# Optimization experiments

Measured on AMD Instinct MI355X. Metric: run time of the kernel, lower is better.

## Reference

```python
import jax, jax.numpy as jnp
import numpy as np

BETA = 1e-8
ALPHA = 0.5
CHOOSE_K = 128
MEMORY_SIZE = 65536
KEY_DIM = 256
BATCH = 1024


def _l2norm(x, axis=-1, eps=1e-12):
    return x / jnp.sqrt(jnp.sum(x * x, axis=axis, keepdims=True) + eps)


def setup_inputs() -> dict:
    key = jax.random.key(0)
    k1, k2, k3 = jax.random.split(key, 3)
    q = _l2norm(jax.random.normal(k1, (BATCH, KEY_DIM), dtype=jnp.float32))
    memory_key = _l2norm(jax.random.normal(k2, (MEMORY_SIZE, KEY_DIM), dtype=jnp.float32))
    # module init: hist[:] = 1e-5; add small random variation so topk is non-degenerate
    memory_hist = 1e-5 + 1e-3 * jax.random.uniform(k3, (MEMORY_SIZE,), dtype=jnp.float32)
    # module init: values = ones, second half zeroed
    memory_values = jnp.concatenate([
        jnp.ones((MEMORY_SIZE // 2,), dtype=jnp.float32),
        jnp.zeros((MEMORY_SIZE - MEMORY_SIZE // 2,), dtype=jnp.float32),
    ])
    return {"q": q, "memory_key": memory_key,
            "memory_hist": memory_hist, "memory_values": memory_values}


def reference(q, memory_key, memory_hist, memory_values):
    # obtain_topk over FULL memory: dense similarity [B, M]
    sims = jnp.matmul(q, memory_key.T)                      # [B, M]
    scores = jnp.exp(sims - 1.0) * (memory_hist + BETA)[None, :]
    _, k_idxs = jax.lax.top_k(scores, CHOOSE_K)             # [B, K]

    # gather reduced memory at topk indices
    red_keys = memory_key[k_idxs]                           # [B, K, D]
    red_hist = memory_hist[k_idxs] * ALPHA                  # [B, K]
    red_vals = memory_values[k_idxs]                        # [B, K]

    # posterior over the K gathered slots
    sim_k = jnp.einsum('bd,bkd->bk', q, red_keys)           # [B, K]
    joint = jnp.exp(sim_k - 1.0) * (red_hist + BETA)        # [B, K]
    posterior = joint / jnp.sum(joint, axis=1, keepdims=True)
    result = jnp.sum(posterior * red_vals, axis=1)          # [B]
    return result
```

## Files before the change

kernel.cpp:

```cpp
#include <hip/hip_runtime.h>

#define BATCH   1024
#define MSIZE   65536
#define KDIM    256
#define CHOOSEK 128
#define SELK    160
#define BETA    1e-8f
#define ALPHA   0.5f
#define KSCALE  426666.7f

typedef short bf16x8 __attribute__((ext_vector_type(8)));
typedef float f32x4  __attribute__((ext_vector_type(4)));

__device__ inline unsigned int pack2bf(float a, float b) {
    unsigned int ua = __float_as_uint(a);
    unsigned int ub = __float_as_uint(b);
    ua += 0x7fffu + ((ua >> 16) & 1u);
    ub += 0x7fffu + ((ub >> 16) & 1u);
    return (ua >> 16) | (ub & 0xffff0000u);
}

#define GLD16(g, l) __builtin_amdgcn_global_load_lds( \
    (const __attribute__((address_space(1))) unsigned int*)(g), \
    (__attribute__((address_space(3))) unsigned int*)(l), 16, 0, 0)

__global__ __launch_bounds__(256)
void convert_kernel(const float* __restrict__ q, const float* __restrict__ key,
                    unsigned short* __restrict__ qb, unsigned short* __restrict__ kb)
{
    const int id = blockIdx.x * 256 + threadIdx.x;
    const float* src; unsigned short* dst; int off;
    if (blockIdx.x < 128) { src = q;   dst = qb; off = id; }
    else                  { src = key; dst = kb; off = id - 32768; }
    const float4* s4 = (const float4*)src;
    float4 a = s4[off * 2];
    float4 b = s4[off * 2 + 1];
    uint4 p = make_uint4(pack2bf(a.x, a.y), pack2bf(a.z, a.w),
                         pack2bf(b.x, b.y), pack2bf(b.z, b.w));
    ((uint4*)dst)[off] = p;
}

__global__ __launch_bounds__(256)
void score_kernel(const unsigned short* __restrict__ qb,
                  const unsigned short* __restrict__ kb,
                  const float* __restrict__ hist,
                  unsigned char* __restrict__ s8)
{
    __shared__ __align__(16) unsigned short As[2][128 * 32];
    __shared__ __align__(16) unsigned short Bs[2][128 * 32];
    const int tid = threadIdx.x;
    const int bid = blockIdx.x;
    const int b0 = ((bid >> 3) & 7) * 128;
    const int n0 = ((bid & 7) + ((bid >> 6) << 3)) * 128;
    const int lane = tid & 63, wave = tid >> 6;
    const int wm = (wave >> 1) * 64, wn = (wave & 1) * 64;
    const int l15 = lane & 15, l4 = lane >> 4;

    f32x4 acc[4][4] = {};

    const int srow = tid >> 2;
    const int seg  = (tid & 3) * 8;
    const unsigned short* gA = qb + (size_t)(b0 + srow) * KDIM + seg;
    const unsigned short* gB = kb + (size_t)(n0 + srow) * KDIM + seg;
    const int lofs = srow * 32 + seg;

    GLD16(gA,             &As[0][lofs]);
    GLD16(gA + 64 * KDIM, &As[0][lofs + 64 * 32]);
    GLD16(gB,             &Bs[0][lofs]);
    GLD16(gB + 64 * KDIM, &Bs[0][lofs + 64 * 32]);
    __syncthreads();

#pragma unroll
    for (int ks = 0; ks < 8; ++ks) {
        const int cur = ks & 1;
        if (ks < 7) {
            const int nxt = cur ^ 1;
            const int ko  = (ks + 1) * 32;
            GLD16(gA + ko,             &As[nxt][lofs]);
            GLD16(gA + ko + 64 * KDIM, &As[nxt][lofs + 64 * 32]);
            GLD16(gB + ko,             &Bs[nxt][lofs]);
            GLD16(gB + ko + 64 * KDIM, &Bs[nxt][lofs + 64 * 32]);
        }
        bf16x8 af[4], bfr[4];
#pragma unroll
        for (int i = 0; i < 4; ++i)
            af[i] = *(const bf16x8*)(&As[cur][(wm + i * 16 + l15) * 32 + l4 * 8]);
#pragma unroll
        for (int j = 0; j < 4; ++j)
            bfr[j] = *(const bf16x8*)(&Bs[cur][(wn + j * 16 + l15) * 32 + l4 * 8]);
#pragma unroll
        for (int i = 0; i < 4; ++i)
#pragma unroll
            for (int j = 0; j < 4; ++j)
                acc[i][j] = __builtin_amdgcn_mfma_f32_16x16x32_bf16(af[i], bfr[j], acc[i][j], 0, 0, 0);
        __syncthreads();
    }

    float hj[4];
#pragma unroll
    for (int j = 0; j < 4; ++j)
        hj[j] = (hist[n0 + wn + j * 16 + l15] + BETA) * KSCALE;
#pragma unroll
    for (int i = 0; i < 4; ++i) {
        const size_t rbase = (size_t)(b0 + wm + i * 16 + l4 * 4) * MSIZE;
#pragma unroll
        for (int j = 0; j < 4; ++j) {
            const int n = n0 + wn + j * 16 + l15;
#pragma unroll
            for (int reg = 0; reg < 4; ++reg) {
                float sc = __expf(acc[i][j][reg] - 1.0f) * hj[j];
                s8[rbase + (size_t)reg * MSIZE + n] = (unsigned char)(int)fminf(sc, 255.0f);
            }
        }
    }
}

__global__ __launch_bounds__(256, 4)
void select_kernel(const float* __restrict__ q,
                   const float* __restrict__ key,
                   const float* __restrict__ hist,
                   const float* __restrict__ vals,
                   const unsigned char* __restrict__ s8,
                   float* __restrict__ out)
{
    const int b   = blockIdx.x;
    const int tid = threadIdx.x;

    __shared__ __align__(16) float qs[KDIM];
    __shared__ unsigned int hcnt[16 * 257];
    __shared__ int   stot[256];
    __shared__ int   scal[2];
    __shared__ int   cidx[1024];
    __shared__ float csc[1024], cjj[1024], cjv[1024];
    __shared__ float wred[8];

    qs[tid] = q[(size_t)b * KDIM + tid];
    const uint4* rowp = reinterpret_cast<const uint4*>(s8 + (size_t)b * MSIZE);
    const int rep = (tid & 15) * 257;

    int H = -1;
    int minb = 128;
    for (;;) {
        for (int i = tid; i < 16 * 257; i += 256) hcnt[i] = 0u;
        if (tid == 0) { scal[0] = -1; scal[1] = 0; }
        __syncthreads();

        for (int i = 0; i < 16; ++i) {
            uint4 v = rowp[i * 256 + tid];
            unsigned int w[4] = {v.x, v.y, v.z, v.w};
#pragma unroll
            for (int k = 0; k < 4; ++k) {
                if (minb == 0 || (w[k] & 0x80808080u)) {
#pragma unroll
                    for (int jj = 0; jj < 4; ++jj) {
                        int bb = (int)((w[k] >> (8 * jj)) & 0xffu);
                        if (bb >= minb) atomicAdd(&hcnt[rep + bb], 1u);
                    }
                }
            }
        }
        __syncthreads();
        { unsigned int t = 0;
#pragma unroll
          for (int k = 0; k < 16; ++k) t += hcnt[k * 257 + tid];
          stot[tid] = (int)t; }
        __syncthreads();

        if (tid < 64) {
            const int l = tid;
            int t0 = stot[l * 4], t1 = stot[l * 4 + 1], t2 = stot[l * 4 + 2], t3 = stot[l * 4 + 3];
            int lsum = t0 + t1 + t2 + t3;
            int s = lsum;
#pragma unroll
            for (int off = 1; off < 64; off <<= 1) {
                int u = __shfl_down(s, off, 64);
                if (l + off < 64) s += u;
            }
            int A  = s - lsum;
            int S3 = A + t3;
            int S2 = S3 + t2;
            int S1 = S2 + t1;
            int S0 = S1 + t0;
            if (S0 >= SELK && S1 < SELK) scal[0] = l * 4 + 0;
            if (S1 >= SELK && S2 < SELK) scal[0] = l * 4 + 1;
            if (S2 >= SELK && S3 < SELK) scal[0] = l * 4 + 2;
            if (S3 >= SELK && A  < SELK) scal[0] = l * 4 + 3;
        }
        __syncthreads();
        H = scal[0];
        __syncthreads();
        if (H >= 0) break;
        minb = 0;
    }

    const unsigned int uH = (unsigned int)H;
    const bool pre = (H >= 128);
    for (int i = 0; i < 16; ++i) {
        uint4 v = rowp[i * 256 + tid];
        const int base = (i * 256 + tid) * 16;
        unsigned int w[4] = {v.x, v.y, v.z, v.w};
#pragma unroll
        for (int k = 0; k < 4; ++k) {
            if (!pre || (w[k] & 0x80808080u)) {
#pragma unroll
                for (int jj = 0; jj < 4; ++jj) {
                    unsigned int bb = (w[k] >> (8 * jj)) & 0xffu;
                    if (bb >= uH) {
                        int p = atomicAdd(&scal[1], 1);
                        if (p < 1024) cidx[p] = base + 4 * k + jj;
                    }
                }
            }
        }
    }
    __syncthreads();
    const int ncand = min(scal[1], 1024);

    const int gid = tid >> 4, gl = tid & 15;
    const float4* q4 = (const float4*)qs;
    for (int i = gid; i < ncand; i += 16) {
        const int idx = cidx[i];
        const float4* kp = (const float4*)(key + (size_t)idx * KDIM);
        float p = 0.f;
#pragma unroll
        for (int u = 0; u < 4; ++u) {
            float4 kk = kp[gl * 4 + u];
            float4 qq = q4[gl * 4 + u];
            p += kk.x * qq.x + kk.y * qq.y + kk.z * qq.z + kk.w * qq.w;
        }
#pragma unroll
        for (int off = 1; off < 16; off <<= 1) p += __shfl_xor(p, off, 64);
        if (gl == 0) {
            float e = expf(p - 1.0f);
            float h = hist[idx];
            csc[i] = e * (h + BETA);
            float j = e * (ALPHA * h + BETA);
            cjj[i] = j;
            cjv[i] = j * vals[idx];
        }
    }
    __syncthreads();

    const int wave = tid >> 6, lane = tid & 63;
    float pn = 0.f, pd = 0.f;
    for (int i = tid; i < ncand; i += 256) {
        float si = csc[i]; int ii = cidx[i]; int rank = 0;
        for (int t = 0; t < ncand; ++t) {
            float st = csc[t];
            rank += (st > si || (st == si && cidx[t] < ii)) ? 1 : 0;
        }
        if (rank < CHOOSEK) { pn += cjv[i]; pd += cjj[i]; }
    }
#pragma unroll
    for (int off = 32; off > 0; off >>= 1) {
        pn += __shfl_xor(pn, off, 64);
        pd += __shfl_xor(pd, off, 64);
    }
    if (lane == 0) { wred[wave] = pn; wred[4 + wave] = pd; }
    __syncthreads();
    if (tid == 0) {
        float n = wred[0] + wred[1] + wred[2] + wred[3];
        float d = wred[4] + wred[5] + wred[6] + wred[7];
        out[b] = n / d;
    }
}

extern "C" void kernel_launch(void* const* d_in, const int* in_sizes, int n_in,
                              void* d_out, int out_size, void* d_ws, size_t ws_size,
                              hipStream_t stream)
{
    (void)in_sizes; (void)n_in; (void)out_size; (void)ws_size;
    const float* q    = (const float*)d_in[0];
    const float* key  = (const float*)d_in[1];
    const float* hist = (const float*)d_in[2];
    const float* vals = (const float*)d_in[3];
    float* out = (float*)d_out;

    unsigned char*  s8 = (unsigned char*)d_ws;
    unsigned short* kb = (unsigned short*)((char*)d_ws + ((size_t)64 << 20));
    unsigned short* qb = (unsigned short*)((char*)d_ws + ((size_t)96 << 20));

    convert_kernel<<<8320, 256, 0, stream>>>(q, key, qb, kb);
    score_kernel<<<4096, 256, 0, stream>>>(qb, kb, hist, s8);
    select_kernel<<<BATCH, 256, 0, stream>>>(q, key, hist, vals, s8, out);
}
```

Before: 210.7 us.

## Load query fragments to registers and swap MFMA operands for packed byte stores

The score GEMM no longer stages the query tile in LDS. Each wave loads its query fragments straight from global memory into registers, double-buffered, and only the key tile goes through LDS. The MFMA operands are swapped so each lane's accumulator holds four consecutive memory slots, which lets the epilogue pack four 8-bit scores into one 32-bit store instead of four scattered byte stores. The hist loads also become float4. This cuts LDS traffic and store transactions, but the per-wave global query loads are redundant across waves and may add latency.

Measured after the change: 249.4 us. +18.4%, slower.

```diff
diff --git a/kernel.cpp b/kernel.cpp
--- a/kernel.cpp
+++ b/kernel.cpp
@@ -46,7 +46,6 @@
                   const float* __restrict__ hist,
                   unsigned char* __restrict__ s8)
 {
-    __shared__ __align__(16) unsigned short As[2][128 * 32];
     __shared__ __align__(16) unsigned short Bs[2][128 * 32];
     const int tid = threadIdx.x;
     const int bid = blockIdx.x;
@@ -60,14 +59,18 @@
 
     const int srow = tid >> 2;
     const int seg  = (tid & 3) * 8;
-    const unsigned short* gA = qb + (size_t)(b0 + srow) * KDIM + seg;
     const unsigned short* gB = kb + (size_t)(n0 + srow) * KDIM + seg;
     const int lofs = srow * 32 + seg;
 
-    GLD16(gA,             &As[0][lofs]);
-    GLD16(gA + 64 * KDIM, &As[0][lofs + 64 * 32]);
+    const unsigned short* gq = qb + (size_t)(b0 + wm + l15) * KDIM + l4 * 8;
+
+    bf16x8 qf[2][4];
+
     GLD16(gB,             &Bs[0][lofs]);
     GLD16(gB + 64 * KDIM, &Bs[0][lofs + 64 * 32]);
+#pragma unroll
+    for (int j = 0; j < 4; ++j)
+        qf[0][j] = *(const bf16x8*)(gq + j * 16 * KDIM);
     __syncthreads();
 
 #pragma unroll
@@ -76,41 +79,44 @@
         if (ks < 7) {
             const int nxt = cur ^ 1;
             const int ko  = (ks + 1) * 32;
-            GLD16(gA + ko,             &As[nxt][lofs]);
-            GLD16(gA + ko + 64 * KDIM, &As[nxt][lofs + 64 * 32]);
+#pragma unroll
+            for (int j = 0; j < 4; ++j)
+                qf[nxt][j] = *(const bf16x8*)(gq + j * 16 * KDIM + ko);
             GLD16(gB + ko,             &Bs[nxt][lofs]);
             GLD16(gB + ko + 64 * KDIM, &Bs[nxt][lofs + 64 * 32]);
         }
-        bf16x8 af[4], bfr[4];
+        bf16x8 kf[4];
 #pragma unroll
         for (int i = 0; i < 4; ++i)
-            af[i] = *(const bf16x8*)(&As[cur][(wm + i * 16 + l15) * 32 + l4 * 8]);
-#pragma unroll
-        for (int j = 0; j < 4; ++j)
-            bfr[j] = *(const bf16x8*)(&Bs[cur][(wn + j * 16 + l15) * 32 + l4 * 8]);
+            kf[i] = *(const bf16x8*)(&Bs[cur][(wn + i * 16 + l15) * 32 + l4 * 8]);
 #pragma unroll
         for (int i = 0; i < 4; ++i)
 #pragma unroll
             for (int j = 0; j < 4; ++j)
-                acc[i][j] = __builtin_amdgcn_mfma_f32_16x16x32_bf16(af[i], bfr[j], acc[i][j], 0, 0, 0);
-        __syncthreads();
-    }
-
-    float hj[4];
-#pragma unroll
-    for (int j = 0; j < 4; ++j)
-        hj[j] = (hist[n0 + wn + j * 16 + l15] + BETA) * KSCALE;
+                acc[i][j] = __builtin_amdgcn_mfma_f32_16x16x32_bf16(kf[i], qf[cur][j], acc[i][j], 0, 0, 0);
+        __syncthreads();
+    }
+
+    float4 hj[4];
 #pragma unroll
     for (int i = 0; i < 4; ++i) {
-        const size_t rbase = (size_t)(b0 + wm + i * 16 + l4 * 4) * MSIZE;
-#pragma unroll
-        for (int j = 0; j < 4; ++j) {
-            const int n = n0 + wn + j * 16 + l15;
+        float4 h = *(const float4*)&hist[n0 + wn + i * 16 + l4 * 4];
+        hj[i] = make_float4((h.x + BETA) * KSCALE, (h.y + BETA) * KSCALE,
+                            (h.z + BETA) * KSCALE, (h.w + BETA) * KSCALE);
+    }
+#pragma unroll
+    for (int j = 0; j < 4; ++j) {
+        const size_t row = (size_t)(b0 + wm + j * 16 + l15) * MSIZE;
+#pragma unroll
+        for (int i = 0; i < 4; ++i) {
+            const float* hv = (const float*)&hj[i];
+            unsigned int pk = 0;
 #pragma unroll
             for (int reg = 0; reg < 4; ++reg) {
-                float sc = __expf(acc[i][j][reg] - 1.0f) * hj[j];
-                s8[rbase + (size_t)reg * MSIZE + n] = (unsigned char)(int)fminf(sc, 255.0f);
-            }
+                float sc = __expf(acc[i][j][reg] - 1.0f) * hv[reg];
+                pk |= (unsigned int)(unsigned char)(int)fminf(sc, 255.0f) << (8 * reg);
+            }
+            *(unsigned int*)(s8 + row + (n0 + wn + i * 16 + l4 * 4)) = pk;
         }
     }
 }
```
